# Kernel optimization log

Hardware: AMD Instinct MI355X
Metric: run time of the kernel (lower is better)

The kernel has to match this reference:

```python
import jax, jax.numpy as jnp
import numpy as np

D_MODEL = 1024
N_HEADS = 16
D_K = D_MODEL // N_HEADS


def setup_inputs() -> dict:
    key = jax.random.key(0)
    ks = jax.random.split(key, 6)
    B, T = 4, 2048
    x = jax.random.normal(ks[0], (B, T, D_MODEL), dtype=jnp.float32)
    # additive causal mask: 0 on/below diagonal, -inf above
    neg = jnp.float32(-1e9)
    attn_mask = jnp.where(jnp.tril(jnp.ones((T, T), dtype=bool)), 0.0, neg).astype(jnp.float32)
    s_in = 1.0 / np.sqrt(D_MODEL)
    Wqkv = jax.random.normal(ks[1], (D_MODEL, 3 * D_MODEL), dtype=jnp.float32) * s_in
    bqkv = jnp.zeros((3 * D_MODEL,), dtype=jnp.float32)
    Wout = jax.random.normal(ks[2], (D_MODEL, D_MODEL), dtype=jnp.float32) * s_in
    bout = jnp.zeros((D_MODEL,), dtype=jnp.float32)
    return {"x": x, "attn_mask": attn_mask, "Wqkv": Wqkv, "bqkv": bqkv,
            "Wout": Wout, "bout": bout}


def reference(x, attn_mask, Wqkv, bqkv, Wout, bout):
    B, T, _ = x.shape
    qkv = x @ Wqkv + bqkv                                  # [B,T,3*D]
    qkv = qkv.reshape(B, T, 3, N_HEADS, D_K)
    qkv = jnp.transpose(qkv, (2, 0, 3, 1, 4))              # [3,B,H,T,d_k]
    q, k, v = qkv[0], qkv[1], qkv[2]
    scores = jnp.einsum('bhqd,bhkd->bhqk', q, k) / jnp.sqrt(jnp.float32(D_K))
    scores = scores + attn_mask                            # broadcast [T,T]
    probs = jax.nn.softmax(scores, axis=-1)
    attn_out = jnp.einsum('bhqk,bhkd->bhqd', probs, v)     # [B,H,T,d_k]
    attn_out = jnp.transpose(attn_out, (0, 2, 1, 3)).reshape(B, T, D_MODEL)
    return attn_out @ Wout + bout
```

## Files before the change

### kernel.cpp

```cpp
#include <hip/hip_runtime.h>
#include <hip/hip_bf16.h>
#include <stdint.h>

typedef __attribute__((ext_vector_type(8))) short short8;
typedef __attribute__((ext_vector_type(4))) short short4v;
typedef __attribute__((ext_vector_type(4))) float f32x4;

#define MFMA16(a, b, c) __builtin_amdgcn_mfma_f32_16x16x32_bf16((a), (b), (c), 0, 0, 0)

static __device__ __forceinline__ short f2bf(float f) {
    union { float f; uint32_t i; } v; v.f = f;
    uint32_t r = v.i + 0x7fffu + ((v.i >> 16) & 1u);
    return (short)(r >> 16);
}

__global__ void conv_f32_bf16(const float* __restrict__ in, short* __restrict__ out, int n4) {
    int i = blockIdx.x * blockDim.x + threadIdx.x;
    int stride = gridDim.x * blockDim.x;
    for (; i < n4; i += stride) {
        f32x4 v = *(const f32x4*)(in + (size_t)i * 4);
        short4v o;
        o[0] = f2bf(v[0]); o[1] = f2bf(v[1]); o[2] = f2bf(v[2]); o[3] = f2bf(v[3]);
        *(short4v*)(out + (size_t)i * 4) = o;
    }
}

__global__ void conv_transpose(const float* __restrict__ W, short* __restrict__ Wt, int R, int C) {
    __shared__ float tile[32][33];
    int c0 = blockIdx.x * 32;
    int r0 = blockIdx.y * 32;
    int tx = threadIdx.x;
    int ty = threadIdx.y;
    for (int j = 0; j < 4; ++j) {
        int r = ty * 4 + j;
        tile[r][tx] = W[(size_t)(r0 + r) * C + c0 + tx];
    }
    __syncthreads();
    for (int j = 0; j < 4; ++j) {
        int c = ty * 4 + j;
        Wt[(size_t)(c0 + c) * R + r0 + tx] = f2bf(tile[tx][c]);
    }
}

__global__ __launch_bounds__(256) void gemm_qkv(
    const short* __restrict__ A, const short* __restrict__ Bt,
    const float* __restrict__ bias,
    short* __restrict__ Qg, short* __restrict__ Kg, short* __restrict__ Vg)
{
    const int K = 1024;
    __shared__ short As[128 * 32];
    __shared__ short Bs[128 * 32];
    const int tid = threadIdx.x, lane = tid & 63, wid = tid >> 6;
    const int wr = wid >> 1, wc = wid & 1;
    const int m0 = blockIdx.y * 128, n0 = blockIdx.x * 128;
    const int l15 = lane & 15, l4 = lane >> 4;

    f32x4 acc[4][4] = {};

    int rowS[2], ugS[2];
    for (int t = 0; t < 2; ++t) {
        int c = tid + t * 256;
        rowS[t] = c >> 2;
        ugS[t] = (c & 3) ^ ((rowS[t] >> 1) & 3);
    }
    int offA[4], offB[4];
    for (int f = 0; f < 4; ++f) {
        int ra = wr * 64 + f * 16 + l15;
        offA[f] = ra * 32 + ((l4 ^ ((ra >> 1) & 3)) * 8);
        int rb = wc * 64 + f * 16 + l15;
        offB[f] = rb * 32 + ((l4 ^ ((rb >> 1) & 3)) * 8);
    }

    for (int k0 = 0; k0 < K; k0 += 32) {
        __syncthreads();
        for (int t = 0; t < 2; ++t) {
            const short* ga = A  + (size_t)(m0 + rowS[t]) * K + k0 + ugS[t] * 8;
            const short* gb = Bt + (size_t)(n0 + rowS[t]) * K + k0 + ugS[t] * 8;
            short* la = As + (t * 256 + wid * 64) * 8;
            short* lb = Bs + (t * 256 + wid * 64) * 8;
            __builtin_amdgcn_global_load_lds((const __attribute__((address_space(1))) void*)ga,
                                             (__attribute__((address_space(3))) void*)la, 16, 0, 0);
            __builtin_amdgcn_global_load_lds((const __attribute__((address_space(1))) void*)gb,
                                             (__attribute__((address_space(3))) void*)lb, 16, 0, 0);
        }
        __syncthreads();
        short8 a[4], b[4];
        for (int f = 0; f < 4; ++f) a[f] = *(const short8*)&As[offA[f]];
        for (int f = 0; f < 4; ++f) b[f] = *(const short8*)&Bs[offB[f]];
        for (int mf = 0; mf < 4; ++mf)
            for (int nf = 0; nf < 4; ++nf)
                acc[mf][nf] = MFMA16(a[mf], b[nf], acc[mf][nf]);
    }

    for (int mf = 0; mf < 4; ++mf) {
        int grow_base = m0 + wr * 64 + mf * 16 + l4 * 4;
        for (int nf = 0; nf < 4; ++nf) {
            int gcol = n0 + wc * 64 + nf * 16 + l15;
            float bb = bias[gcol];
            int which = gcol >> 10, rem = gcol & 1023;
            int h = rem >> 6, d = rem & 63;
            for (int r = 0; r < 4; ++r) {
                int grow = grow_base + r;
                int b = grow >> 11, t = grow & 2047;
                int bh = (b << 4) + h;
                float val = acc[mf][nf][r] + bb;
                if (which == 0) val *= 0.125f;
                short bv = f2bf(val);
                if (which == 0)      Qg[((size_t)bh * 2048 + t) * 64 + d] = bv;
                else if (which == 1) Kg[((size_t)bh * 2048 + t) * 64 + d] = bv;
                else                 Vg[((size_t)bh * 64 + d) * 2048 + t] = bv;
            }
        }
    }
}

__global__ __launch_bounds__(256) void attn_kernel(
    const short* __restrict__ Qg, const short* __restrict__ Kg, const short* __restrict__ Vg,
    short* __restrict__ AO)
{
    __shared__ short Ps[4][2][16 * 72];
    const int tid = threadIdx.x, lane = tid & 63, wid = tid >> 6;
    const int l15 = lane & 15, l4 = lane >> 4;
    const int bp = blockIdx.x;
    const int xcd = bp & 7, slot = bp >> 3;
    const int bh = xcd * 8 + (slot >> 3);
    const int iblk = slot & 7;
    const int pr = iblk * 4 + wid;
    const short* Qh = Qg + (size_t)bh * 2048 * 64;
    const short* Kh = Kg + (size_t)bh * 2048 * 64;
    const short* Vh = Vg + (size_t)bh * 64 * 2048;
    const int b = bh >> 4, head = bh & 15;
    short* Pw[2] = { &Ps[wid][0][0], &Ps[wid][1][0] };

    for (int half = 0; half < 2; ++half) {
        const int s = half ? (63 - pr) : pr;
        const int q0 = s * 32;
        const int ntiles = (s >> 1) + 1;

        short8 qf[2][2];
        #pragma unroll
        for (int h = 0; h < 2; ++h)
            #pragma unroll
            for (int c = 0; c < 2; ++c)
                qf[h][c] = *(const short8*)&Qh[(size_t)(q0 + h * 16 + l15) * 64 + c * 32 + l4 * 8];

        f32x4 o[2][4] = {};
        float lsum[2][4] = {};

        for (int j = 0; j < ntiles; ++j) {
            const int kv0 = j * 64;
            const bool diag = (j == ntiles - 1);
            short8 kb[4][2], vb[4][2];
            #pragma unroll
            for (int kf = 0; kf < 4; ++kf)
                #pragma unroll
                for (int c = 0; c < 2; ++c)
                    kb[kf][c] = *(const short8*)&Kh[(size_t)(kv0 + kf * 16 + l15) * 64 + c * 32 + l4 * 8];
            #pragma unroll
            for (int df = 0; df < 4; ++df)
                #pragma unroll
                for (int c = 0; c < 2; ++c)
                    vb[df][c] = *(const short8*)&Vh[(size_t)(df * 16 + l15) * 2048 + kv0 + c * 32 + l4 * 8];

            #pragma unroll
            for (int h = 0; h < 2; ++h) {
                f32x4 sf[4];
                #pragma unroll
                for (int kf = 0; kf < 4; ++kf) {
                    f32x4 z = {};
                    z = MFMA16(qf[h][0], kb[kf][0], z);
                    z = MFMA16(qf[h][1], kb[kf][1], z);
                    sf[kf] = z;
                }
                short* P = Pw[h];
                float ts[4] = {};
                const int gq = q0 + h * 16 + l4 * 4;
                #pragma unroll
                for (int kf = 0; kf < 4; ++kf) {
                    const int gk = kv0 + kf * 16 + l15;
                    #pragma unroll
                    for (int r = 0; r < 4; ++r) {
                        float v = sf[kf][r];
                        if (diag && gk > gq + r) v = -1e9f;
                        float pp = __expf(v);
                        ts[r] += pp;
                        P[(l4 * 4 + r) * 72 + kf * 16 + l15] = f2bf(pp);
                    }
                }
                #pragma unroll
                for (int mk = 1; mk <= 8; mk <<= 1)
                    #pragma unroll
                    for (int r = 0; r < 4; ++r)
                        ts[r] += __shfl_xor(ts[r], mk, 64);
                #pragma unroll
                for (int r = 0; r < 4; ++r) lsum[h][r] += ts[r];

                asm volatile("s_waitcnt lgkmcnt(0)" ::: "memory");
                short8 pa0 = *(const short8*)&P[l15 * 72 + l4 * 8];
                short8 pa1 = *(const short8*)&P[l15 * 72 + 32 + l4 * 8];
                #pragma unroll
                for (int df = 0; df < 4; ++df) {
                    o[h][df] = MFMA16(pa0, vb[df][0], o[h][df]);
                    o[h][df] = MFMA16(pa1, vb[df][1], o[h][df]);
                }
            }
        }

        #pragma unroll
        for (int h = 0; h < 2; ++h)
            #pragma unroll
            for (int r = 0; r < 4; ++r) {
                float inv = 1.0f / lsum[h][r];
                size_t grow = (size_t)b * 2048 + q0 + h * 16 + l4 * 4 + r;
                #pragma unroll
                for (int df = 0; df < 4; ++df)
                    AO[grow * 1024 + head * 64 + df * 16 + l15] = f2bf(o[h][df][r] * inv);
            }
    }
}

__global__ __launch_bounds__(256) void gemm_out(
    const short* __restrict__ A, const short* __restrict__ Bt,
    const float* __restrict__ bias, float* __restrict__ out)
{
    const int K = 1024;
    __shared__ short As[128 * 32];
    __shared__ short Bs[128 * 32];
    const int tid = threadIdx.x, lane = tid & 63, wid = tid >> 6;
    const int wr = wid >> 1, wc = wid & 1;
    const int m0 = blockIdx.y * 128, n0 = blockIdx.x * 128;
    const int l15 = lane & 15, l4 = lane >> 4;

    f32x4 acc[4][4] = {};

    int rowS[2], ugS[2];
    for (int t = 0; t < 2; ++t) {
        int c = tid + t * 256;
        rowS[t] = c >> 2;
        ugS[t] = (c & 3) ^ ((rowS[t] >> 1) & 3);
    }
    int offA[4], offB[4];
    for (int f = 0; f < 4; ++f) {
        int ra = wr * 64 + f * 16 + l15;
        offA[f] = ra * 32 + ((l4 ^ ((ra >> 1) & 3)) * 8);
        int rb = wc * 64 + f * 16 + l15;
        offB[f] = rb * 32 + ((l4 ^ ((rb >> 1) & 3)) * 8);
    }

    for (int k0 = 0; k0 < K; k0 += 32) {
        __syncthreads();
        for (int t = 0; t < 2; ++t) {
            const short* ga = A  + (size_t)(m0 + rowS[t]) * K + k0 + ugS[t] * 8;
            const short* gb = Bt + (size_t)(n0 + rowS[t]) * K + k0 + ugS[t] * 8;
            short* la = As + (t * 256 + wid * 64) * 8;
            short* lb = Bs + (t * 256 + wid * 64) * 8;
            __builtin_amdgcn_global_load_lds((const __attribute__((address_space(1))) void*)ga,
                                             (__attribute__((address_space(3))) void*)la, 16, 0, 0);
            __builtin_amdgcn_global_load_lds((const __attribute__((address_space(1))) void*)gb,
                                             (__attribute__((address_space(3))) void*)lb, 16, 0, 0);
        }
        __syncthreads();
        short8 a[4], b[4];
        for (int f = 0; f < 4; ++f) a[f] = *(const short8*)&As[offA[f]];
        for (int f = 0; f < 4; ++f) b[f] = *(const short8*)&Bs[offB[f]];
        for (int mf = 0; mf < 4; ++mf)
            for (int nf = 0; nf < 4; ++nf)
                acc[mf][nf] = MFMA16(a[mf], b[nf], acc[mf][nf]);
    }

    for (int mf = 0; mf < 4; ++mf) {
        int grow_base = m0 + wr * 64 + mf * 16 + l4 * 4;
        for (int nf = 0; nf < 4; ++nf) {
            int gcol = n0 + wc * 64 + nf * 16 + l15;
            float bb = bias[gcol];
            for (int r = 0; r < 4; ++r) {
                int grow = grow_base + r;
                out[(size_t)grow * 1024 + gcol] = acc[mf][nf][r] + bb;
            }
        }
    }
}

extern "C" void kernel_launch(void* const* d_in, const int* in_sizes, int n_in,
                              void* d_out, int out_size, void* d_ws, size_t ws_size,
                              hipStream_t stream) {
    (void)in_sizes; (void)n_in; (void)out_size; (void)ws_size;
    const float* x    = (const float*)d_in[0];
    const float* Wqkv = (const float*)d_in[2];
    const float* bqkv = (const float*)d_in[3];
    const float* Wout = (const float*)d_in[4];
    const float* bout = (const float*)d_in[5];
    float* out = (float*)d_out;

    char* ws = (char*)d_ws;
    short* xb    = (short*)(ws);
    short* WqkvT = (short*)(ws + (16ull << 20));
    short* WoutT = (short*)(ws + (22ull << 20));
    short* Qg    = (short*)(ws + (24ull << 20));
    short* Kg    = (short*)(ws + (40ull << 20));
    short* Vg    = (short*)(ws + (56ull << 20));
    short* AO    = xb;

    conv_f32_bf16<<<2048, 256, 0, stream>>>(x, xb, 8192 * 1024 / 4);
    conv_transpose<<<dim3(3072 / 32, 1024 / 32), dim3(32, 8), 0, stream>>>(Wqkv, WqkvT, 1024, 3072);
    conv_transpose<<<dim3(1024 / 32, 1024 / 32), dim3(32, 8), 0, stream>>>(Wout, WoutT, 1024, 1024);
    gemm_qkv<<<dim3(24, 64), 256, 0, stream>>>(xb, WqkvT, bqkv, Qg, Kg, Vg);
    attn_kernel<<<512, 256, 0, stream>>>(Qg, Kg, Vg, AO);
    gemm_out<<<dim3(8, 64), 256, 0, stream>>>(AO, WoutT, bout, out);
}
```

Baseline: 346.5 us.

## Double-buffer K/V register loads and defer row-sum reduction in attention

The attention kernel now prefetches the next K/V tile into a second register set while computing the current tile, alternating buffers A and B, and specializes the diagonal-mask path to the final tile only. The per-tile cross-lane shuffle reduction of softmax sums is deferred to a single reduction after the KV loop. Launch bounds add a minimum of 2 blocks per CU. The aim is to hide global load latency and remove shuffle work, at the cost of extra registers and code size, which may hurt occupancy or cause spilling.

```diff
diff --git a/kernel.cpp b/kernel.cpp
--- a/kernel.cpp
+++ b/kernel.cpp
@@ -114,7 +114,53 @@
     }
 }
 
-__global__ __launch_bounds__(256) void attn_kernel(
+#define LOAD_KV(KB, VB, KV0) do {                                                               \
+    _Pragma("unroll")                                                                           \
+    for (int kf_ = 0; kf_ < 4; ++kf_) {                                                         \
+        KB[kf_][0] = *(const short8*)&Kh[(size_t)((KV0) + kf_ * 16 + l15) * 64 + l4 * 8];       \
+        KB[kf_][1] = *(const short8*)&Kh[(size_t)((KV0) + kf_ * 16 + l15) * 64 + 32 + l4 * 8];  \
+        VB[kf_][0] = *(const short8*)&Vh[(size_t)(kf_ * 16 + l15) * 2048 + (KV0) + l4 * 8];     \
+        VB[kf_][1] = *(const short8*)&Vh[(size_t)(kf_ * 16 + l15) * 2048 + (KV0) + 32 + l4 * 8];\
+    }                                                                                           \
+} while (0)
+
+#define COMPUTE_TILE(KB, VB, KV0, DIAG) do {                                                    \
+    _Pragma("unroll")                                                                           \
+    for (int h_ = 0; h_ < 2; ++h_) {                                                            \
+        f32x4 sf_[4];                                                                           \
+        _Pragma("unroll")                                                                       \
+        for (int kf_ = 0; kf_ < 4; ++kf_) {                                                     \
+            f32x4 z_ = {};                                                                      \
+            z_ = MFMA16(qf[h_][0], KB[kf_][0], z_);                                             \
+            z_ = MFMA16(qf[h_][1], KB[kf_][1], z_);                                             \
+            sf_[kf_] = z_;                                                                      \
+        }                                                                                       \
+        short* P_ = Pw[h_];                                                                     \
+        const int gq_ = q0 + h_ * 16 + l4 * 4;                                                  \
+        _Pragma("unroll")                                                                       \
+        for (int kf_ = 0; kf_ < 4; ++kf_) {                                                     \
+            const int gk_ = (KV0) + kf_ * 16 + l15;                                             \
+            _Pragma("unroll")                                                                   \
+            for (int r_ = 0; r_ < 4; ++r_) {                                                    \
+                float v_ = sf_[kf_][r_];                                                        \
+                if (DIAG && gk_ > gq_ + r_) v_ = -1e9f;                                         \
+                float pp_ = __expf(v_);                                                         \
+                lsum[h_][r_] += pp_;                                                            \
+                P_[(l4 * 4 + r_) * 72 + kf_ * 16 + l15] = f2bf(pp_);                            \
+            }                                                                                   \
+        }                                                                                       \
+        asm volatile("s_waitcnt lgkmcnt(0)" ::: "memory");                                      \
+        short8 pa0_ = *(const short8*)&P_[l15 * 72 + l4 * 8];                                   \
+        short8 pa1_ = *(const short8*)&P_[l15 * 72 + 32 + l4 * 8];                              \
+        _Pragma("unroll")                                                                       \
+        for (int df_ = 0; df_ < 4; ++df_) {                                                     \
+            o[h_][df_] = MFMA16(pa0_, VB[df_][0], o[h_][df_]);                                  \
+            o[h_][df_] = MFMA16(pa1_, VB[df_][1], o[h_][df_]);                                  \
+        }                                                                                       \
+    }                                                                                           \
+} while (0)
+
+__global__ __launch_bounds__(256, 2) void attn_kernel(
     const short* __restrict__ Qg, const short* __restrict__ Kg, const short* __restrict__ Vg,
     short* __restrict__ AO)
 {
@@ -135,7 +181,7 @@
     for (int half = 0; half < 2; ++half) {
         const int s = half ? (63 - pr) : pr;
         const int q0 = s * 32;
-        const int ntiles = (s >> 1) + 1;
+        const int nt = (s >> 1) + 1;
 
         short8 qf[2][2];
         #pragma unroll
@@ -147,64 +193,27 @@
         f32x4 o[2][4] = {};
         float lsum[2][4] = {};
 
-        for (int j = 0; j < ntiles; ++j) {
-            const int kv0 = j * 64;
-            const bool diag = (j == ntiles - 1);
-            short8 kb[4][2], vb[4][2];
+        short8 kbA[4][2], vbA[4][2], kbB[4][2], vbB[4][2];
+        LOAD_KV(kbA, vbA, 0);
+        int j = 0;
+        for (;;) {
+            if (j == nt - 1) { COMPUTE_TILE(kbA, vbA, j * 64, true); break; }
+            LOAD_KV(kbB, vbB, (j + 1) * 64);
+            COMPUTE_TILE(kbA, vbA, j * 64, false);
+            ++j;
+            if (j == nt - 1) { COMPUTE_TILE(kbB, vbB, j * 64, true); break; }
+            LOAD_KV(kbA, vbA, (j + 1) * 64);
+            COMPUTE_TILE(kbB, vbB, j * 64, false);
+            ++j;
+        }
+
+        #pragma unroll
+        for (int mk = 1; mk <= 8; mk <<= 1)
             #pragma unroll
-            for (int kf = 0; kf < 4; ++kf)
+            for (int h = 0; h < 2; ++h)
                 #pragma unroll
-                for (int c = 0; c < 2; ++c)
-                    kb[kf][c] = *(const short8*)&Kh[(size_t)(kv0 + kf * 16 + l15) * 64 + c * 32 + l4 * 8];
-            #pragma unroll
-            for (int df = 0; df < 4; ++df)
-                #pragma unroll
-                for (int c = 0; c < 2; ++c)
-                    vb[df][c] = *(const short8*)&Vh[(size_t)(df * 16 + l15) * 2048 + kv0 + c * 32 + l4 * 8];
-
-            #pragma unroll
-            for (int h = 0; h < 2; ++h) {
-                f32x4 sf[4];
-                #pragma unroll
-                for (int kf = 0; kf < 4; ++kf) {
-                    f32x4 z = {};
-                    z = MFMA16(qf[h][0], kb[kf][0], z);
-                    z = MFMA16(qf[h][1], kb[kf][1], z);
-                    sf[kf] = z;
-                }
-                short* P = Pw[h];
-                float ts[4] = {};
-                const int gq = q0 + h * 16 + l4 * 4;
-                #pragma unroll
-                for (int kf = 0; kf < 4; ++kf) {
-                    const int gk = kv0 + kf * 16 + l15;
-                    #pragma unroll
-                    for (int r = 0; r < 4; ++r) {
-                        float v = sf[kf][r];
-                        if (diag && gk > gq + r) v = -1e9f;
-                        float pp = __expf(v);
-                        ts[r] += pp;
-                        P[(l4 * 4 + r) * 72 + kf * 16 + l15] = f2bf(pp);
-                    }
-                }
-                #pragma unroll
-                for (int mk = 1; mk <= 8; mk <<= 1)
-                    #pragma unroll
-                    for (int r = 0; r < 4; ++r)
-                        ts[r] += __shfl_xor(ts[r], mk, 64);
-                #pragma unroll
-                for (int r = 0; r < 4; ++r) lsum[h][r] += ts[r];
-
-                asm volatile("s_waitcnt lgkmcnt(0)" ::: "memory");
-                short8 pa0 = *(const short8*)&P[l15 * 72 + l4 * 8];
-                short8 pa1 = *(const short8*)&P[l15 * 72 + 32 + l4 * 8];
-                #pragma unroll
-                for (int df = 0; df < 4; ++df) {
-                    o[h][df] = MFMA16(pa0, vb[df][0], o[h][df]);
-                    o[h][df] = MFMA16(pa1, vb[df][1], o[h][df]);
-                }
-            }
-        }
+                for (int r = 0; r < 4; ++r)
+                    lsum[h][r] += __shfl_xor(lsum[h][r], mk, 64);
 
         #pragma unroll
         for (int h = 0; h < 2; ++h)
```

Result: slower. 377.8 us (+9.1%).

## Split attention KV range across wave pairs and combine partials in LDS

Applied to the files above, without the earlier changes.

Each query strip is now handled by two waves that each process half of the KV tiles. The second wave writes its partial output and row sums to shared memory, and the first wave adds them in and writes the normalized result. The grid doubles to 1024 blocks to raise parallelism and shorten the critical path of long causal rows. The per-tile row-sum shuffle reduction is also deferred to a single reduction at the end. The cost is extra LDS traffic, two block barriers per half, and idle waves during the combine step.

```diff
diff --git a/kernel.cpp b/kernel.cpp
--- a/kernel.cpp
+++ b/kernel.cpp
@@ -119,23 +119,29 @@
     short* __restrict__ AO)
 {
     __shared__ short Ps[4][2][16 * 72];
+    __shared__ float Comb[2][64][41];
     const int tid = threadIdx.x, lane = tid & 63, wid = tid >> 6;
     const int l15 = lane & 15, l4 = lane >> 4;
     const int bp = blockIdx.x;
     const int xcd = bp & 7, slot = bp >> 3;
-    const int bh = xcd * 8 + (slot >> 3);
-    const int iblk = slot & 7;
-    const int pr = iblk * 4 + wid;
+    const int bh = xcd * 8 + (slot >> 4);
+    const int iblk = slot & 15;
+    const int pairi = iblk * 2 + (wid >> 1);
+    const int kh = wid & 1;
     const short* Qh = Qg + (size_t)bh * 2048 * 64;
     const short* Kh = Kg + (size_t)bh * 2048 * 64;
     const short* Vh = Vg + (size_t)bh * 64 * 2048;
     const int b = bh >> 4, head = bh & 15;
     short* Pw[2] = { &Ps[wid][0][0], &Ps[wid][1][0] };
+    float* cb = &Comb[wid >> 1][lane][0];
 
     for (int half = 0; half < 2; ++half) {
-        const int s = half ? (63 - pr) : pr;
+        const int s = half ? (63 - pairi) : pairi;
         const int q0 = s * 32;
-        const int ntiles = (s >> 1) + 1;
+        const int nt = (s >> 1) + 1;
+        const int nA = (nt + 1) >> 1;
+        const int jbeg = kh ? nA : 0;
+        const int jend = kh ? nt : nA;
 
         short8 qf[2][2];
         #pragma unroll
@@ -147,9 +153,9 @@
         f32x4 o[2][4] = {};
         float lsum[2][4] = {};
 
-        for (int j = 0; j < ntiles; ++j) {
+        for (int j = jbeg; j < jend; ++j) {
             const int kv0 = j * 64;
-            const bool diag = (j == ntiles - 1);
+            const bool diag = (j == nt - 1);
             short8 kb[4][2], vb[4][2];
             #pragma unroll
             for (int kf = 0; kf < 4; ++kf)
@@ -173,7 +179,6 @@
                     sf[kf] = z;
                 }
                 short* P = Pw[h];
-                float ts[4] = {};
                 const int gq = q0 + h * 16 + l4 * 4;
                 #pragma unroll
                 for (int kf = 0; kf < 4; ++kf) {
@@ -183,18 +188,10 @@
                         float v = sf[kf][r];
                         if (diag && gk > gq + r) v = -1e9f;
                         float pp = __expf(v);
-                        ts[r] += pp;
+                        lsum[h][r] += pp;
                         P[(l4 * 4 + r) * 72 + kf * 16 + l15] = f2bf(pp);
                     }
                 }
-                #pragma unroll
-                for (int mk = 1; mk <= 8; mk <<= 1)
-                    #pragma unroll
-                    for (int r = 0; r < 4; ++r)
-                        ts[r] += __shfl_xor(ts[r], mk, 64);
-                #pragma unroll
-                for (int r = 0; r < 4; ++r) lsum[h][r] += ts[r];
-
                 asm volatile("s_waitcnt lgkmcnt(0)" ::: "memory");
                 short8 pa0 = *(const short8*)&P[l15 * 72 + l4 * 8];
                 short8 pa1 = *(const short8*)&P[l15 * 72 + 32 + l4 * 8];
@@ -206,16 +203,53 @@
             }
         }
 
-        #pragma unroll
-        for (int h = 0; h < 2; ++h)
-            #pragma unroll
-            for (int r = 0; r < 4; ++r) {
-                float inv = 1.0f / lsum[h][r];
-                size_t grow = (size_t)b * 2048 + q0 + h * 16 + l4 * 4 + r;
+        if (kh) {
+            #pragma unroll
+            for (int h = 0; h < 2; ++h)
                 #pragma unroll
                 for (int df = 0; df < 4; ++df)
-                    AO[grow * 1024 + head * 64 + df * 16 + l15] = f2bf(o[h][df][r] * inv);
-            }
+                    #pragma unroll
+                    for (int r = 0; r < 4; ++r)
+                        cb[(h * 4 + df) * 4 + r] = o[h][df][r];
+            #pragma unroll
+            for (int h = 0; h < 2; ++h)
+                #pragma unroll
+                for (int r = 0; r < 4; ++r)
+                    cb[32 + h * 4 + r] = lsum[h][r];
+        }
+        __syncthreads();
+        if (!kh) {
+            #pragma unroll
+            for (int h = 0; h < 2; ++h)
+                #pragma unroll
+                for (int df = 0; df < 4; ++df)
+                    #pragma unroll
+                    for (int r = 0; r < 4; ++r)
+                        o[h][df][r] += cb[(h * 4 + df) * 4 + r];
+            #pragma unroll
+            for (int h = 0; h < 2; ++h)
+                #pragma unroll
+                for (int r = 0; r < 4; ++r)
+                    lsum[h][r] += cb[32 + h * 4 + r];
+            #pragma unroll
+            for (int mk = 1; mk <= 8; mk <<= 1)
+                #pragma unroll
+                for (int h = 0; h < 2; ++h)
+                    #pragma unroll
+                    for (int r = 0; r < 4; ++r)
+                        lsum[h][r] += __shfl_xor(lsum[h][r], mk, 64);
+            #pragma unroll
+            for (int h = 0; h < 2; ++h)
+                #pragma unroll
+                for (int r = 0; r < 4; ++r) {
+                    float inv = 1.0f / lsum[h][r];
+                    size_t grow = (size_t)b * 2048 + q0 + h * 16 + l4 * 4 + r;
+                    #pragma unroll
+                    for (int df = 0; df < 4; ++df)
+                        AO[grow * 1024 + head * 64 + df * 16 + l15] = f2bf(o[h][df][r] * inv);
+                }
+        }
+        __syncthreads();
     }
 }
 
@@ -305,6 +339,6 @@
     conv_transpose<<<dim3(3072 / 32, 1024 / 32), dim3(32, 8), 0, stream>>>(Wqkv, WqkvT, 1024, 3072);
     conv_transpose<<<dim3(1024 / 32, 1024 / 32), dim3(32, 8), 0, stream>>>(Wout, WoutT, 1024, 1024);
     gemm_qkv<<<dim3(24, 64), 256, 0, stream>>>(xb, WqkvT, bqkv, Qg, Kg, Vg);
-    attn_kernel<<<512, 256, 0, stream>>>(Qg, Kg, Vg, AO);
+    attn_kernel<<<1024, 256, 0, stream>>>(Qg, Kg, Vg, AO);
     gemm_out<<<dim3(8, 64), 256, 0, stream>>>(AO, WoutT, bout, out);
 }
```

After: 349.1 us. About the same (+0.8%).

## Keep softmax probabilities in registers via transposed QK^T MFMA and permuted V layout

Applied to the files above, without the earlier changes.

Computes the score tile as K·Q^T so each lane holds a column of probabilities, packs them to bf16 with v_cvt_pk_bf16_f32, and feeds them straight into the PV MFMA as the A operand. This removes the LDS round-trip and wait for P. V is stored with a permuted key order within each 64-key block so its fragment layout matches the register-resident P. The Q scale now folds in log2(e) so exp2f replaces __expf. Row sums are reduced once after the loop instead of with per-tile shuffles.

```diff
diff --git a/kernel.cpp b/kernel.cpp
--- a/kernel.cpp
+++ b/kernel.cpp
@@ -5,6 +5,7 @@
 typedef __attribute__((ext_vector_type(8))) short short8;
 typedef __attribute__((ext_vector_type(4))) short short4v;
 typedef __attribute__((ext_vector_type(4))) float f32x4;
+typedef __attribute__((ext_vector_type(4))) int   i32x4;
 
 #define MFMA16(a, b, c) __builtin_amdgcn_mfma_f32_16x16x32_bf16((a), (b), (c), 0, 0, 0)
 
@@ -12,6 +13,12 @@
     union { float f; uint32_t i; } v; v.f = f;
     uint32_t r = v.i + 0x7fffu + ((v.i >> 16) & 1u);
     return (short)(r >> 16);
+}
+
+static __device__ __forceinline__ int cvtpk(float a, float b) {
+    int r;
+    asm("v_cvt_pk_bf16_f32 %0, %1, %2" : "=v"(r) : "v"(a), "v"(b));
+    return r;
 }
 
 __global__ void conv_f32_bf16(const float* __restrict__ in, short* __restrict__ out, int n4) {
@@ -104,11 +111,15 @@
                 int b = grow >> 11, t = grow & 2047;
                 int bh = (b << 4) + h;
                 float val = acc[mf][nf][r] + bb;
-                if (which == 0) val *= 0.125f;
+                if (which == 0) val *= 0.18033688011112042f;
                 short bv = f2bf(val);
                 if (which == 0)      Qg[((size_t)bh * 2048 + t) * 64 + d] = bv;
                 else if (which == 1) Kg[((size_t)bh * 2048 + t) * 64 + d] = bv;
-                else                 Vg[((size_t)bh * 64 + d) * 2048 + t] = bv;
+                else {
+                    int k6 = t & 63;
+                    int pos = (k6 & 32) + ((k6 & 12) << 1) + ((k6 & 16) >> 2) + (k6 & 3);
+                    Vg[((size_t)bh * 64 + d) * 2048 + (t & ~63) + pos] = bv;
+                }
             }
         }
     }
@@ -118,7 +129,6 @@
     const short* __restrict__ Qg, const short* __restrict__ Kg, const short* __restrict__ Vg,
     short* __restrict__ AO)
 {
-    __shared__ short Ps[4][2][16 * 72];
     const int tid = threadIdx.x, lane = tid & 63, wid = tid >> 6;
     const int l15 = lane & 15, l4 = lane >> 4;
     const int bp = blockIdx.x;
@@ -130,12 +140,11 @@
     const short* Kh = Kg + (size_t)bh * 2048 * 64;
     const short* Vh = Vg + (size_t)bh * 64 * 2048;
     const int b = bh >> 4, head = bh & 15;
-    short* Pw[2] = { &Ps[wid][0][0], &Ps[wid][1][0] };
 
     for (int half = 0; half < 2; ++half) {
         const int s = half ? (63 - pr) : pr;
         const int q0 = s * 32;
-        const int ntiles = (s >> 1) + 1;
+        const int nt = (s >> 1) + 1;
 
         short8 qf[2][2];
         #pragma unroll
@@ -145,11 +154,11 @@
                 qf[h][c] = *(const short8*)&Qh[(size_t)(q0 + h * 16 + l15) * 64 + c * 32 + l4 * 8];
 
         f32x4 o[2][4] = {};
-        float lsum[2][4] = {};
-
-        for (int j = 0; j < ntiles; ++j) {
+        float lsum[2] = { 0.f, 0.f };
+
+        for (int j = 0; j < nt; ++j) {
             const int kv0 = j * 64;
-            const bool diag = (j == ntiles - 1);
+            const bool diag = (j == nt - 1);
             short8 kb[4][2], vb[4][2];
             #pragma unroll
             for (int kf = 0; kf < 4; ++kf)
@@ -168,49 +177,48 @@
                 #pragma unroll
                 for (int kf = 0; kf < 4; ++kf) {
                     f32x4 z = {};
-                    z = MFMA16(qf[h][0], kb[kf][0], z);
-                    z = MFMA16(qf[h][1], kb[kf][1], z);
+                    z = MFMA16(kb[kf][0], qf[h][0], z);
+                    z = MFMA16(kb[kf][1], qf[h][1], z);
                     sf[kf] = z;
                 }
-                short* P = Pw[h];
-                float ts[4] = {};
-                const int gq = q0 + h * 16 + l4 * 4;
+                const int gq = q0 + h * 16 + l15;
+                int w[4][2];
                 #pragma unroll
                 for (int kf = 0; kf < 4; ++kf) {
-                    const int gk = kv0 + kf * 16 + l15;
+                    float pf[4];
                     #pragma unroll
                     for (int r = 0; r < 4; ++r) {
                         float v = sf[kf][r];
-                        if (diag && gk > gq + r) v = -1e9f;
-                        float pp = __expf(v);
-                        ts[r] += pp;
-                        P[(l4 * 4 + r) * 72 + kf * 16 + l15] = f2bf(pp);
+                        if (diag && (kv0 + kf * 16 + l4 * 4 + r) > gq) v = -1e9f;
+                        float pp = exp2f(v);
+                        lsum[h] += pp;
+                        pf[r] = pp;
                     }
+                    w[kf][0] = cvtpk(pf[0], pf[1]);
+                    w[kf][1] = cvtpk(pf[2], pf[3]);
                 }
-                #pragma unroll
-                for (int mk = 1; mk <= 8; mk <<= 1)
-                    #pragma unroll
-                    for (int r = 0; r < 4; ++r)
-                        ts[r] += __shfl_xor(ts[r], mk, 64);
-                #pragma unroll
-                for (int r = 0; r < 4; ++r) lsum[h][r] += ts[r];
-
-                asm volatile("s_waitcnt lgkmcnt(0)" ::: "memory");
-                short8 pa0 = *(const short8*)&P[l15 * 72 + l4 * 8];
-                short8 pa1 = *(const short8*)&P[l15 * 72 + 32 + l4 * 8];
+                union { i32x4 i; short8 s8; } pa0, pa1;
+                pa0.i[0] = w[0][0]; pa0.i[1] = w[0][1]; pa0.i[2] = w[1][0]; pa0.i[3] = w[1][1];
+                pa1.i[0] = w[2][0]; pa1.i[1] = w[2][1]; pa1.i[2] = w[3][0]; pa1.i[3] = w[3][1];
                 #pragma unroll
                 for (int df = 0; df < 4; ++df) {
-                    o[h][df] = MFMA16(pa0, vb[df][0], o[h][df]);
-                    o[h][df] = MFMA16(pa1, vb[df][1], o[h][df]);
+                    o[h][df] = MFMA16(pa0.s8, vb[df][0], o[h][df]);
+                    o[h][df] = MFMA16(pa1.s8, vb[df][1], o[h][df]);
                 }
             }
         }
 
         #pragma unroll
+        for (int h = 0; h < 2; ++h) {
+            lsum[h] += __shfl_xor(lsum[h], 16, 64);
+            lsum[h] += __shfl_xor(lsum[h], 32, 64);
+        }
+
+        #pragma unroll
         for (int h = 0; h < 2; ++h)
             #pragma unroll
             for (int r = 0; r < 4; ++r) {
-                float inv = 1.0f / lsum[h][r];
+                float inv = 1.0f / __shfl(lsum[h], l4 * 4 + r, 64);
                 size_t grow = (size_t)b * 2048 + q0 + h * 16 + l4 * 4 + r;
                 #pragma unroll
                 for (int df = 0; df < 4; ++df)
```

Result: no change. 341.9 us (-1.3%).
